# Kernel optimization log

Hardware: AMD Instinct MI355X
Metric: run time of the kernel (lower is better)

The kernel has to match this reference:

```python
import jax, jax.numpy as jnp
import numpy as np

B, S, D = 2, 2048, 2048
H, KVH = 16, 4
HD = D // H            # 128
KVD = KVH * HD         # 512
ROPE_BASE = 10000.0
EPS = 1e-6


def setup_inputs() -> dict:
    key = jax.random.key(0)
    k0, k1, k2, k3, k4, k5 = jax.random.split(key, 6)
    x = jax.random.normal(k0, (B, S, D), dtype=jnp.float32)
    # torch Linear weights are [out_features, in_features]
    Wq = jax.random.normal(k1, (D, D), dtype=jnp.float32) * 0.02
    Wk = jax.random.normal(k2, (KVD, D), dtype=jnp.float32) * 0.02
    Wv = jax.random.normal(k3, (KVD, D), dtype=jnp.float32) * 0.02
    Wproj = jax.random.normal(k4, (D, D), dtype=jnp.float32) * 0.02
    q_gain = jnp.ones((H,), dtype=jnp.float32)
    return {"x": x, "Wq": Wq, "Wk": Wk, "Wv": Wv, "Wproj": Wproj, "q_gain": q_gain}


def _rms_norm(t):
    return t * jax.lax.rsqrt(jnp.mean(t * t, axis=-1, keepdims=True) + EPS)


def _rope_tables(seqlen, dtype):
    half = HD // 2
    inv_freq = 1.0 / (ROPE_BASE ** (jnp.arange(0, HD, 2, dtype=jnp.float32) / HD))
    freqs = jnp.outer(jnp.arange(seqlen, dtype=jnp.float32), inv_freq)  # [S, half]
    return jnp.cos(freqs).astype(dtype)[None, None], jnp.sin(freqs).astype(dtype)[None, None]


def _apply_rope(t, cos, sin):
    half = t.shape[-1] // 2
    t1, t2 = t[..., :half], t[..., half:]
    return jnp.concatenate((t1 * cos + t2 * sin, -t1 * sin + t2 * cos), axis=-1)


def reference(x, Wq, Wk, Wv, Wproj, q_gain):
    bsz, seqlen, _ = x.shape
    # QKV projections (F.linear: x @ W.T)
    q = jnp.einsum('bsd,ed->bse', x, Wq).reshape(bsz, seqlen, H, HD).transpose(0, 2, 1, 3)
    k = jnp.einsum('bsd,ed->bse', x, Wk).reshape(bsz, seqlen, KVH, HD).transpose(0, 2, 1, 3)
    v = jnp.einsum('bsd,ed->bse', x, Wv).reshape(bsz, seqlen, KVH, HD).transpose(0, 2, 1, 3)
    # QK RMS-norm
    q = _rms_norm(q)
    k = _rms_norm(k)
    # RoPE
    cos, sin = _rope_tables(seqlen, q.dtype)
    q = _apply_rope(q, cos, sin)
    k = _apply_rope(k, cos, sin)
    # per-head query gain
    q = q * q_gain.astype(q.dtype)[None, :, None, None]
    # GQA: repeat_interleave kv heads
    rep = H // KVH
    k = jnp.repeat(k, rep, axis=1)
    v = jnp.repeat(v, rep, axis=1)
    # causal SDPA
    scale = 1.0 / jnp.sqrt(jnp.asarray(HD, dtype=q.dtype))
    scores = jnp.einsum('bhqd,bhkd->bhqk', q, k) * scale
    causal = jnp.tril(jnp.ones((seqlen, seqlen), dtype=bool))
    scores = jnp.where(causal[None, None], scores, jnp.finfo(scores.dtype).min)
    attn = jax.nn.softmax(scores, axis=-1)
    y = jnp.einsum('bhqk,bhkd->bhqd', attn, v)
    y = y.transpose(0, 2, 1, 3).reshape(bsz, seqlen, H * HD)
    return jnp.einsum('bse,de->bsd', y, Wproj)
```

## Files before the change

kernel.cpp:

```cpp
#include <hip/hip_runtime.h>


typedef __bf16 bf16x8 __attribute__((ext_vector_type(8)));
typedef float  f32x4  __attribute__((ext_vector_type(4)));

#define LOG2E 1.4426950408889634f
#define FIXC  16.59099297022308f

__device__ __forceinline__ float b2f(ushort h) {
  return __builtin_bit_cast(float, ((unsigned)h) << 16);
}
__device__ __forceinline__ ushort f2b(float f) {
  unsigned u = __builtin_bit_cast(unsigned, f);
  return (ushort)((u + 0x7fffu + ((u >> 16) & 1u)) >> 16);
}
__device__ __forceinline__ void async16(ushort* lds, const ushort* g) {
  __builtin_amdgcn_global_load_lds(
      (const __attribute__((address_space(1))) unsigned int*)(const void*)g,
      (__attribute__((address_space(3))) unsigned int*)(void*)lds, 16, 0, 0);
}
__device__ __forceinline__ f32x4 mfma16(bf16x8 a, bf16x8 b, f32x4 c) {
  return __builtin_amdgcn_mfma_f32_16x16x32_bf16(a, b, c, 0, 0, 0);
}

__global__ __launch_bounds__(256) void castk(const float* __restrict__ in,
                                             ushort* __restrict__ out) {
  int i = blockIdx.x * 256 + threadIdx.x;
  float4 v = ((const float4*)in)[i];
  ushort4 o = make_ushort4(f2b(v.x), f2b(v.y), f2b(v.z), f2b(v.w));
  ((ushort4*)out)[i] = o;
}

__global__ void rope_tables(float* __restrict__ cosT, float* __restrict__ sinT) {
  int s = blockIdx.x;
  int i = threadIdx.x;
  float invf = exp2f(-(float)i * (13.287712379549449f / 64.0f));
  float ang = (float)s * invf;
  float sn, cs;
  sincosf(ang, &sn, &cs);
  cosT[s * 64 + i] = cs;
  sinT[s * 64 + i] = sn;
}

__device__ __forceinline__ void store_c(float* C, size_t idx, float v) { C[idx] = v; }
__device__ __forceinline__ void store_c(ushort* C, size_t idx, float v) { C[idx] = f2b(v); }

template <typename TOUT>
__global__ __launch_bounds__(256) void gemm_bt(const ushort* __restrict__ A,
                                               const ushort* __restrict__ Bw,
                                               TOUT* __restrict__ C,
                                               int M, int N, int K) {
  __shared__ __align__(16) ushort As[128 * 32];
  __shared__ __align__(16) ushort Bs[128 * 32];
  int tid = threadIdx.x;
  int lane = tid & 63, wid = tid >> 6;
  int gx = gridDim.x;
  int nwg = gx * gridDim.y;
  int lid = blockIdx.y * gx + blockIdx.x;
  int cpx = nwg >> 3;
  int swz = (lid & 7) * cpx + (lid >> 3);
  int bm = swz / gx, bn = swz % gx;
  int wr = wid >> 1, wc = wid & 1;
  int lr = lane & 15, kg = lane >> 4;
  f32x4 z = {0.f, 0.f, 0.f, 0.f};
  f32x4 acc[4][4];
#pragma unroll
  for (int m = 0; m < 4; ++m)
#pragma unroll
    for (int n = 0; n < 4; ++n) acc[m][n] = z;

  const ushort* Ab = A + (size_t)bm * 128 * K;
  const ushort* Bb = Bw + (size_t)bn * 128 * K;
  int c0 = tid, c1 = tid + 256;

  for (int k0 = 0; k0 < K; k0 += 32) {
    async16(&As[c0 * 8], Ab + (size_t)(c0 >> 2) * K + k0 + (c0 & 3) * 8);
    async16(&As[c1 * 8], Ab + (size_t)(c1 >> 2) * K + k0 + (c1 & 3) * 8);
    async16(&Bs[c0 * 8], Bb + (size_t)(c0 >> 2) * K + k0 + (c0 & 3) * 8);
    async16(&Bs[c1 * 8], Bb + (size_t)(c1 >> 2) * K + k0 + (c1 & 3) * 8);
    __syncthreads();
    bf16x8 af[4], bfr[4];
#pragma unroll
    for (int m = 0; m < 4; ++m)
      af[m] = *(const bf16x8*)&As[(wr * 64 + m * 16 + lr) * 32 + kg * 8];
#pragma unroll
    for (int n = 0; n < 4; ++n)
      bfr[n] = *(const bf16x8*)&Bs[(wc * 64 + n * 16 + lr) * 32 + kg * 8];
#pragma unroll
    for (int m = 0; m < 4; ++m)
#pragma unroll
      for (int n = 0; n < 4; ++n)
        acc[m][n] = mfma16(af[m], bfr[n], acc[m][n]);
    __syncthreads();
  }
#pragma unroll
  for (int m = 0; m < 4; ++m)
#pragma unroll
    for (int n = 0; n < 4; ++n)
#pragma unroll
      for (int r4 = 0; r4 < 4; ++r4) {
        int row = bm * 128 + wr * 64 + m * 16 + kg * 4 + r4;
        int col = bn * 128 + wc * 64 + n * 16 + lr;
        store_c(C, (size_t)row * N + col, acc[m][n][r4]);
      }
}

__global__ __launch_bounds__(256) void rms_rope(ushort* __restrict__ qkv,
                                                const float* __restrict__ gain,
                                                const float* __restrict__ cosT,
                                                const float* __restrict__ sinT) {
  int w = blockIdx.x * 4 + (threadIdx.x >> 6);
  int lane = threadIdx.x & 63;
  int token = w / 20, slot = w % 20;
  int s = token & 2047;
  ushort* p = qkv + (size_t)token * 3072 +
              (slot < 16 ? slot * 128 : 2048 + (slot - 16) * 128);
  float t1 = b2f(p[lane]);
  float t2 = b2f(p[lane + 64]);
  float ss = t1 * t1 + t2 * t2;
#pragma unroll
  for (int off = 32; off >= 1; off >>= 1) ss += __shfl_xor(ss, off);
  float r = rsqrtf(ss * (1.0f / 128.0f) + 1e-6f);
  t1 *= r; t2 *= r;
  float c = cosT[s * 64 + lane], sn = sinT[s * 64 + lane];
  float o1 = t1 * c + t2 * sn;
  float o2 = t2 * c - t1 * sn;
  if (slot < 16) {
    float g = gain[slot] * 0.08838834764831845f;
    o1 *= g; o2 *= g;
  }
  p[lane] = f2b(o1);
  p[lane + 64] = f2b(o2);
}

__global__ __launch_bounds__(512) void attn_fwd(const ushort* __restrict__ qkv,
                                                ushort* __restrict__ y) {
  __shared__ __align__(16) ushort LDS[32768];
  ushort* Vt = LDS + 16384;
  ushort* Ps = LDS + 24576;
  ushort* Qst = LDS + 8192;

  int tid = threadIdx.x, lane = tid & 63, wid = tid >> 6;
  int lr = lane & 15, kg = lane >> 4;
  int i = blockIdx.x, bh = blockIdx.y;
  int b = bh >> 4, h = bh & 15, kvh = h >> 2;
  int lo = i, hi = 31 - i;
  size_t tokbase = (size_t)b * 2048;

  bool isHi = (wid < 4);
  int wq = isHi ? wid : (wid - 4);
  int ldsrow0 = (isHi ? 0 : 64) + wq * 16;
  int qtile = isHi ? hi : lo;
  int qbase = qtile * 64 + wq * 16;
  int nt = hi + 1;

#pragma unroll
  for (int it = 0; it < 4; ++it) {
    int c = it * 512 + tid;
    int r = c >> 4, a = c & 15;
    int asrc = a ^ (r & 7);
    int qrow = (r < 64) ? hi * 64 + r : lo * 64 + (r - 64);
    async16(&Qst[c * 8], qkv + (tokbase + qrow) * 3072 + h * 128 + asrc * 8);
  }
#pragma unroll
  for (int i2 = 0; i2 < 2; ++i2) {
    int c = i2 * 512 + tid;
    int r = c >> 4, a = c & 15;
    int asrc = a ^ (r & 7);
    async16(&LDS[c * 8], qkv + (tokbase + r) * 3072 + 2048 + kvh * 128 + asrc * 8);
  }
  int vkv0 = tid >> 4, vd0 = (tid & 15) * 8;
  uint4 va = *(const uint4*)(qkv + (tokbase + vkv0) * 3072 + 2560 + kvh * 128 + vd0);
  uint4 vb_ = *(const uint4*)(qkv + (tokbase + 32 + vkv0) * 3072 + 2560 + kvh * 128 + vd0);

  __syncthreads();

  bf16x8 qf[4];
#pragma unroll
  for (int kk = 0; kk < 4; ++kk) {
    int r = ldsrow0 + lr;
    int a = (kk * 4 + kg) ^ (r & 7);
    qf[kk] = *(const bf16x8*)&Qst[r * 128 + a * 8];
  }
  __syncthreads();

  f32x4 z = {0.f, 0.f, 0.f, 0.f};
  f32x4 acc_y[8];
#pragma unroll
  for (int n2 = 0; n2 < 8; ++n2) acc_y[n2] = z;
  float lsum[4] = {0.f, 0.f, 0.f, 0.f};

  for (int t = 0; t < nt; ++t) {
    ushort* kb = LDS + ((t & 1) ? 8192 : 0);
#pragma unroll
    for (int i2 = 0; i2 < 2; ++i2) {
      union { uint4 u; ushort s[8]; } vv;
      vv.u = i2 ? vb_ : va;
      int kv = i2 * 32 + vkv0;
#pragma unroll
      for (int j = 0; j < 8; ++j) {
        int d = vd0 + j;
        int sw = (d & 7) ^ ((d >> 3) & 7);
        Vt[d * 64 + (kv ^ (sw << 3))] = vv.s[j];
      }
    }
    __syncthreads();

    if (t + 1 < nt) {
      ushort* kn = LDS + (((t + 1) & 1) ? 8192 : 0);
      int ktn = (t + 1) * 64;
#pragma unroll
      for (int i2 = 0; i2 < 2; ++i2) {
        int c = i2 * 512 + tid;
        int r = c >> 4, a = c & 15;
        int asrc = a ^ (r & 7);
        async16(&kn[c * 8],
                qkv + (tokbase + ktn + r) * 3072 + 2048 + kvh * 128 + asrc * 8);
      }
      va  = *(const uint4*)(qkv + (tokbase + ktn + vkv0) * 3072 + 2560 + kvh * 128 + vd0);
      vb_ = *(const uint4*)(qkv + (tokbase + ktn + 32 + vkv0) * 3072 + 2560 + kvh * 128 + vd0);
    }

    bool act = isHi || (t <= lo);
    if (act) {
      int kt = t * 64;
      f32x4 sc[4];
#pragma unroll
      for (int n = 0; n < 4; ++n) sc[n] = z;
      __builtin_amdgcn_s_setprio(1);
#pragma unroll
      for (int n = 0; n < 4; ++n)
#pragma unroll
        for (int kk = 0; kk < 4; ++kk) {
          int r = n * 16 + lr;
          int a = (kk * 4 + kg) ^ (r & 7);
          bf16x8 kf = *(const bf16x8*)&kb[r * 128 + a * 8];
          sc[n] = mfma16(qf[kk], kf, sc[n]);
        }
      __builtin_amdgcn_s_setprio(0);
      if (t == qtile) {
#pragma unroll
        for (int n = 0; n < 4; ++n)
#pragma unroll
          for (int r4 = 0; r4 < 4; ++r4) {
            int kvg = kt + n * 16 + lr;
            int qg = qbase + kg * 4 + r4;
            if (kvg > qg) sc[n][r4] = -1.0e30f;
          }
      }
#pragma unroll
      for (int n = 0; n < 4; ++n)
#pragma unroll
        for (int r4 = 0; r4 < 4; ++r4) {
          float pv = __builtin_amdgcn_exp2f(fmaf(sc[n][r4], LOG2E, -FIXC));
          lsum[r4] += pv;
          int q = ldsrow0 + kg * 4 + r4;
          int col = n * 16 + lr;
          Ps[q * 64 + (col ^ ((q & 7) << 3))] = f2b(pv);
        }
      bf16x8 pa[2];
#pragma unroll
      for (int kk2 = 0; kk2 < 2; ++kk2) {
        int q = ldsrow0 + lr;
        pa[kk2] = *(const bf16x8*)&Ps[q * 64 + ((kk2 * 32 + kg * 8) ^ ((q & 7) << 3))];
      }
      __builtin_amdgcn_s_setprio(1);
#pragma unroll
      for (int n2 = 0; n2 < 8; ++n2) {
        int d = n2 * 16 + lr;
        int sw = (d & 7) ^ ((d >> 3) & 7);
#pragma unroll
        for (int kk2 = 0; kk2 < 2; ++kk2) {
          bf16x8 vb = *(const bf16x8*)&Vt[d * 64 + ((kk2 * 32 + kg * 8) ^ (sw << 3))];
          acc_y[n2] = mfma16(pa[kk2], vb, acc_y[n2]);
        }
      }
      __builtin_amdgcn_s_setprio(0);
    }
    __syncthreads();
  }

#pragma unroll
  for (int off = 1; off < 16; off <<= 1)
#pragma unroll
    for (int r4 = 0; r4 < 4; ++r4) lsum[r4] += __shfl_xor(lsum[r4], off);
  float rl[4];
#pragma unroll
  for (int r4 = 0; r4 < 4; ++r4) rl[r4] = 1.0f / lsum[r4];
#pragma unroll
  for (int n2 = 0; n2 < 8; ++n2)
#pragma unroll
    for (int r4 = 0; r4 < 4; ++r4) {
      int q = qbase + kg * 4 + r4;
      float v = acc_y[n2][r4] * rl[r4];
      y[(tokbase + q) * 2048 + h * 128 + n2 * 16 + lr] = f2b(v);
    }
}

extern "C" void kernel_launch(void* const* d_in, const int* in_sizes, int n_in,
                              void* d_out, int out_size, void* d_ws, size_t ws_size,
                              hipStream_t stream) {
  const float* x  = (const float*)d_in[0];
  const float* Wq = (const float*)d_in[1];
  const float* Wk = (const float*)d_in[2];
  const float* Wv = (const float*)d_in[3];
  const float* Wp = (const float*)d_in[4];
  const float* qg = (const float*)d_in[5];
  float* out = (float*)d_out;

  char* w = (char*)d_ws;
  ushort* xb    = (ushort*)w; w += (size_t)4096 * 2048 * 2;
  ushort* wqkv  = (ushort*)w; w += (size_t)3072 * 2048 * 2;
  ushort* wproj = (ushort*)w; w += (size_t)2048 * 2048 * 2;
  ushort* qkv   = (ushort*)w; w += (size_t)4096 * 3072 * 2;
  ushort* yb    = (ushort*)w; w += (size_t)4096 * 2048 * 2;
  float*  cosT  = (float*)w;  w += (size_t)2048 * 64 * 4;
  float*  sinT  = (float*)w;  w += (size_t)2048 * 64 * 4;

  castk<<<8192, 256, 0, stream>>>(x, xb);
  castk<<<4096, 256, 0, stream>>>(Wq, wqkv);
  castk<<<1024, 256, 0, stream>>>(Wk, wqkv + (size_t)2048 * 2048);
  castk<<<1024, 256, 0, stream>>>(Wv, wqkv + (size_t)2560 * 2048);
  castk<<<4096, 256, 0, stream>>>(Wp, wproj);
  rope_tables<<<2048, 64, 0, stream>>>(cosT, sinT);

  gemm_bt<ushort><<<dim3(24, 32), 256, 0, stream>>>(xb, wqkv, qkv, 4096, 3072, 2048);
  rms_rope<<<20480, 256, 0, stream>>>(qkv, qg, cosT, sinT);
  attn_fwd<<<dim3(16, 32), 512, 0, stream>>>(qkv, yb);
  gemm_bt<float><<<dim3(16, 32), 256, 0, stream>>>(yb, wproj, out, 4096, 2048, 2048);
}
```

Before: 364.6 us.

## Split high-tile KV work across idle waves and widen GEMM K-step with swizzle

In attention, once the low query tile has finished its KV range, its waves switch to the high query tile and take the odd KV tiles of each pair in parallel with the other waves. The two partial outputs and row sums are then merged through LDS, which balances work across all eight waves instead of leaving half of them idle. The GEMM now stages 64-wide K chunks with an XOR-swizzled LDS layout, halving the number of barriers per K and reducing bank conflicts. The cost is more LDS (two V buffers), more registers for a second accumulator set, and a merge step at the end. Q is now loaded straight from global memory instead of being staged through LDS.

New measurement: 344.1 us. 1.06x faster.

```diff
diff --git a/kernel.cpp b/kernel.cpp
--- a/kernel.cpp
+++ b/kernel.cpp
@@ -50,8 +50,8 @@
                                                const ushort* __restrict__ Bw,
                                                TOUT* __restrict__ C,
                                                int M, int N, int K) {
-  __shared__ __align__(16) ushort As[128 * 32];
-  __shared__ __align__(16) ushort Bs[128 * 32];
+  __shared__ __align__(16) ushort As[128 * 64];
+  __shared__ __align__(16) ushort Bs[128 * 64];
   int tid = threadIdx.x;
   int lane = tid & 63, wid = tid >> 6;
   int gx = gridDim.x;
@@ -71,26 +71,41 @@
 
   const ushort* Ab = A + (size_t)bm * 128 * K;
   const ushort* Bb = Bw + (size_t)bn * 128 * K;
-  int c0 = tid, c1 = tid + 256;
-
-  for (int k0 = 0; k0 < K; k0 += 32) {
-    async16(&As[c0 * 8], Ab + (size_t)(c0 >> 2) * K + k0 + (c0 & 3) * 8);
-    async16(&As[c1 * 8], Ab + (size_t)(c1 >> 2) * K + k0 + (c1 & 3) * 8);
-    async16(&Bs[c0 * 8], Bb + (size_t)(c0 >> 2) * K + k0 + (c0 & 3) * 8);
-    async16(&Bs[c1 * 8], Bb + (size_t)(c1 >> 2) * K + k0 + (c1 & 3) * 8);
-    __syncthreads();
-    bf16x8 af[4], bfr[4];
+
+  for (int k0 = 0; k0 < K; k0 += 64) {
+#pragma unroll
+    for (int p = 0; p < 4; ++p) {
+      int c = p * 256 + tid;
+      int r = c >> 3, ch = c & 7;
+      int chs = ch ^ (r & 7);
+      async16(&As[c * 8], Ab + (size_t)r * K + k0 + chs * 8);
+      async16(&Bs[c * 8], Bb + (size_t)r * K + k0 + chs * 8);
+    }
+    __syncthreads();
+    bf16x8 af[4][2], bfr[4][2];
 #pragma unroll
     for (int m = 0; m < 4; ++m)
-      af[m] = *(const bf16x8*)&As[(wr * 64 + m * 16 + lr) * 32 + kg * 8];
+#pragma unroll
+      for (int kk = 0; kk < 2; ++kk) {
+        int r = wr * 64 + m * 16 + lr;
+        int a = (kk * 4 + kg) ^ (r & 7);
+        af[m][kk] = *(const bf16x8*)&As[r * 64 + a * 8];
+      }
 #pragma unroll
     for (int n = 0; n < 4; ++n)
-      bfr[n] = *(const bf16x8*)&Bs[(wc * 64 + n * 16 + lr) * 32 + kg * 8];
+#pragma unroll
+      for (int kk = 0; kk < 2; ++kk) {
+        int r = wc * 64 + n * 16 + lr;
+        int a = (kk * 4 + kg) ^ (r & 7);
+        bfr[n][kk] = *(const bf16x8*)&Bs[r * 64 + a * 8];
+      }
 #pragma unroll
     for (int m = 0; m < 4; ++m)
 #pragma unroll
       for (int n = 0; n < 4; ++n)
-        acc[m][n] = mfma16(af[m], bfr[n], acc[m][n]);
+#pragma unroll
+        for (int kk = 0; kk < 2; ++kk)
+          acc[m][n] = mfma16(af[m][kk], bfr[n][kk], acc[m][n]);
     __syncthreads();
   }
 #pragma unroll
@@ -133,12 +148,73 @@
   p[lane + 64] = f2b(o2);
 }
 
+__device__ __forceinline__ void compute_tile(
+    const ushort* __restrict__ kb, const ushort* __restrict__ vt,
+    ushort* __restrict__ Ps, const bf16x8 (&qf)[4],
+    f32x4 (&acc)[8], float (&ls)[4],
+    int lr, int kg, int ldsrow0, bool domask, int kt, int qr0) {
+  f32x4 z = {0.f, 0.f, 0.f, 0.f};
+  f32x4 sc[4];
+#pragma unroll
+  for (int n = 0; n < 4; ++n) sc[n] = z;
+  __builtin_amdgcn_s_setprio(1);
+#pragma unroll
+  for (int n = 0; n < 4; ++n)
+#pragma unroll
+    for (int kk = 0; kk < 4; ++kk) {
+      int r = n * 16 + lr;
+      int a = (kk * 4 + kg) ^ (r & 7);
+      bf16x8 kf = *(const bf16x8*)&kb[r * 128 + a * 8];
+      sc[n] = mfma16(qf[kk], kf, sc[n]);
+    }
+  __builtin_amdgcn_s_setprio(0);
+  if (domask) {
+#pragma unroll
+    for (int n = 0; n < 4; ++n)
+#pragma unroll
+      for (int r4 = 0; r4 < 4; ++r4) {
+        int kvg = kt + n * 16 + lr;
+        int qg = qr0 + kg * 4 + r4;
+        if (kvg > qg) sc[n][r4] = -1.0e30f;
+      }
+  }
+#pragma unroll
+  for (int n = 0; n < 4; ++n)
+#pragma unroll
+    for (int r4 = 0; r4 < 4; ++r4) {
+      float pv = __builtin_amdgcn_exp2f(fmaf(sc[n][r4], LOG2E, -FIXC));
+      ls[r4] += pv;
+      int q = ldsrow0 + kg * 4 + r4;
+      int col = n * 16 + lr;
+      Ps[q * 64 + (col ^ ((q & 7) << 3))] = f2b(pv);
+    }
+  bf16x8 pa0, pa1;
+  {
+    int q = ldsrow0 + lr;
+    pa0 = *(const bf16x8*)&Ps[q * 64 + ((kg * 8) ^ ((q & 7) << 3))];
+    pa1 = *(const bf16x8*)&Ps[q * 64 + ((32 + kg * 8) ^ ((q & 7) << 3))];
+  }
+  __builtin_amdgcn_s_setprio(1);
+#pragma unroll
+  for (int n2 = 0; n2 < 8; ++n2) {
+    int d = n2 * 16 + lr;
+    int sw = (d & 7) ^ ((d >> 3) & 7);
+    bf16x8 v0 = *(const bf16x8*)&vt[d * 64 + ((kg * 8) ^ (sw << 3))];
+    acc[n2] = mfma16(pa0, v0, acc[n2]);
+    bf16x8 v1 = *(const bf16x8*)&vt[d * 64 + ((32 + kg * 8) ^ (sw << 3))];
+    acc[n2] = mfma16(pa1, v1, acc[n2]);
+  }
+  __builtin_amdgcn_s_setprio(0);
+}
+
 __global__ __launch_bounds__(512) void attn_fwd(const ushort* __restrict__ qkv,
                                                 ushort* __restrict__ y) {
-  __shared__ __align__(16) ushort LDS[32768];
-  ushort* Vt = LDS + 16384;
-  ushort* Ps = LDS + 24576;
-  ushort* Qst = LDS + 8192;
+  __shared__ __align__(16) ushort LDS[40960];
+  ushort* K0 = LDS;
+  ushort* K1 = LDS + 8192;
+  ushort* V0 = LDS + 16384;
+  ushort* V1 = LDS + 24576;
+  ushort* Ps = LDS + 32768;
 
   int tid = threadIdx.x, lane = tid & 63, wid = tid >> 6;
   int lr = lane & 15, kg = lane >> 4;
@@ -147,154 +223,157 @@
   int lo = i, hi = 31 - i;
   size_t tokbase = (size_t)b * 2048;
 
-  bool isHi = (wid < 4);
-  int wq = isHi ? wid : (wid - 4);
-  int ldsrow0 = (isHi ? 0 : 64) + wq * 16;
-  int qtile = isHi ? hi : lo;
-  int qbase = qtile * 64 + wq * 16;
-  int nt = hi + 1;
-
-#pragma unroll
-  for (int it = 0; it < 4; ++it) {
-    int c = it * 512 + tid;
-    int r = c >> 4, a = c & 15;
-    int asrc = a ^ (r & 7);
-    int qrow = (r < 64) ? hi * 64 + r : lo * 64 + (r - 64);
-    async16(&Qst[c * 8], qkv + (tokbase + qrow) * 3072 + h * 128 + asrc * 8);
-  }
-#pragma unroll
-  for (int i2 = 0; i2 < 2; ++i2) {
-    int c = i2 * 512 + tid;
-    int r = c >> 4, a = c & 15;
-    int asrc = a ^ (r & 7);
-    async16(&LDS[c * 8], qkv + (tokbase + r) * 3072 + 2048 + kvh * 128 + asrc * 8);
-  }
+  bool w03 = (wid < 4);
+  int g = wid & 3;
+  int ldsrow0 = (w03 ? 0 : 64) + g * 16;
+  int qr0A = (w03 ? hi : lo) * 64 + g * 16;
+  int qr0B = hi * 64 + g * 16;
+
   int vkv0 = tid >> 4, vd0 = (tid & 15) * 8;
-  uint4 va = *(const uint4*)(qkv + (tokbase + vkv0) * 3072 + 2560 + kvh * 128 + vd0);
-  uint4 vb_ = *(const uint4*)(qkv + (tokbase + 32 + vkv0) * 3072 + 2560 + kvh * 128 + vd0);
-
+  uint4 va, vb_;
+
+#define STAGE_K(BUF, T)                                                      \
+  {                                                                          \
+    _Pragma("unroll") for (int i2 = 0; i2 < 2; ++i2) {                       \
+      int c = i2 * 512 + tid;                                                \
+      int r = c >> 4, a = c & 15;                                            \
+      int asrc = a ^ (r & 7);                                                \
+      async16(&(BUF)[c * 8],                                                 \
+              qkv + (tokbase + (size_t)(T) * 64 + r) * 3072 + 2048 +         \
+                  kvh * 128 + asrc * 8);                                     \
+    }                                                                        \
+  }
+#define LOAD_V(T)                                                            \
+  {                                                                          \
+    va = *(const uint4*)(qkv + (tokbase + (size_t)(T) * 64 + vkv0) * 3072 +  \
+                         2560 + kvh * 128 + vd0);                            \
+    vb_ = *(const uint4*)(qkv +                                              \
+                          (tokbase + (size_t)(T) * 64 + 32 + vkv0) * 3072 +  \
+                          2560 + kvh * 128 + vd0);                           \
+  }
+#define WRITE_V(VB)                                                          \
+  {                                                                          \
+    union { uint4 u; ushort s[8]; } vv0, vv1;                                \
+    vv0.u = va; vv1.u = vb_;                                                 \
+    _Pragma("unroll") for (int j = 0; j < 8; ++j) {                          \
+      int d = vd0 + j;                                                       \
+      int sw = (d & 7) ^ ((d >> 3) & 7);                                     \
+      (VB)[d * 64 + (vkv0 ^ (sw << 3))] = vv0.s[j];                          \
+      (VB)[d * 64 + ((32 + vkv0) ^ (sw << 3))] = vv1.s[j];                   \
+    }                                                                        \
+  }
+
+  bf16x8 qf[4];
+#pragma unroll
+  for (int kk = 0; kk < 4; ++kk)
+    qf[kk] = *(const bf16x8*)(qkv + (tokbase + qr0A + lr) * 3072 + h * 128 +
+                              (kk * 4 + kg) * 8);
+
+  f32x4 z = {0.f, 0.f, 0.f, 0.f};
+  f32x4 acc_y[8], acc2[8];
+#pragma unroll
+  for (int n2 = 0; n2 < 8; ++n2) { acc_y[n2] = z; acc2[n2] = z; }
+  float lsum[4] = {0.f, 0.f, 0.f, 0.f};
+  float lsum2[4] = {0.f, 0.f, 0.f, 0.f};
+
+  STAGE_K(K0, 0);
+  LOAD_V(0);
+
+  for (int s = 0; s <= lo; ++s) {
+    ushort* kb = (s & 1) ? K1 : K0;
+    ushort* vt = (s & 1) ? V1 : V0;
+    WRITE_V(vt);
+    __syncthreads();
+    if (s < lo) {
+      STAGE_K(((s & 1) ? K0 : K1), s + 1);
+      LOAD_V(s + 1);
+    }
+    compute_tile(kb, vt, Ps, qf, acc_y, lsum, lr, kg, ldsrow0,
+                 (!w03 && s == lo), s * 64, qr0A);
+    __syncthreads();
+  }
+
+  if (!w03) {
+#pragma unroll
+    for (int kk = 0; kk < 4; ++kk)
+      qf[kk] = *(const bf16x8*)(qkv + (tokbase + qr0B + lr) * 3072 + h * 128 +
+                                (kk * 4 + kg) * 8);
+  }
+
+  int mmax = 15 - i;
+  for (int m = 0; m <= mmax; ++m) {
+    int t0 = lo + 1 + 2 * m;
+    bool has1 = (t0 + 1 <= hi);
+    LOAD_V(t0);
+    STAGE_K(K0, t0);
+    if (has1) STAGE_K(K1, t0 + 1);
+    WRITE_V(V0);
+    if (has1) {
+      LOAD_V(t0 + 1);
+      WRITE_V(V1);
+    }
+    __syncthreads();
+    if (w03) {
+      compute_tile(K0, V0, Ps, qf, acc_y, lsum, lr, kg, ldsrow0,
+                   (t0 == hi), t0 * 64, qr0B);
+    } else if (has1) {
+      compute_tile(K1, V1, Ps, qf, acc2, lsum2, lr, kg, ldsrow0,
+                   false, (t0 + 1) * 64, qr0B);
+    }
+    __syncthreads();
+  }
+
+#pragma unroll
+  for (int off = 1; off < 16; off <<= 1)
+#pragma unroll
+    for (int r4 = 0; r4 < 4; ++r4) {
+      lsum[r4] += __shfl_xor(lsum[r4], off);
+      lsum2[r4] += __shfl_xor(lsum2[r4], off);
+    }
+
+  float* scf = (float*)LDS;
+  float* scl = (float*)(LDS + 16384);
+  if (!w03) {
+#pragma unroll
+    for (int n2 = 0; n2 < 8; ++n2)
+#pragma unroll
+      for (int r4 = 0; r4 < 4; ++r4)
+        scf[(g * 16 + kg * 4 + r4) * 128 + n2 * 16 + lr] = acc2[n2][r4];
+#pragma unroll
+    for (int r4 = 0; r4 < 4; ++r4)
+      if (lr == r4) scl[g * 16 + kg * 4 + r4] = lsum2[r4];
+  }
   __syncthreads();
 
-  bf16x8 qf[4];
-#pragma unroll
-  for (int kk = 0; kk < 4; ++kk) {
-    int r = ldsrow0 + lr;
-    int a = (kk * 4 + kg) ^ (r & 7);
-    qf[kk] = *(const bf16x8*)&Qst[r * 128 + a * 8];
-  }
-  __syncthreads();
-
-  f32x4 z = {0.f, 0.f, 0.f, 0.f};
-  f32x4 acc_y[8];
-#pragma unroll
-  for (int n2 = 0; n2 < 8; ++n2) acc_y[n2] = z;
-  float lsum[4] = {0.f, 0.f, 0.f, 0.f};
-
-  for (int t = 0; t < nt; ++t) {
-    ushort* kb = LDS + ((t & 1) ? 8192 : 0);
-#pragma unroll
-    for (int i2 = 0; i2 < 2; ++i2) {
-      union { uint4 u; ushort s[8]; } vv;
-      vv.u = i2 ? vb_ : va;
-      int kv = i2 * 32 + vkv0;
-#pragma unroll
-      for (int j = 0; j < 8; ++j) {
-        int d = vd0 + j;
-        int sw = (d & 7) ^ ((d >> 3) & 7);
-        Vt[d * 64 + (kv ^ (sw << 3))] = vv.s[j];
-      }
-    }
-    __syncthreads();
-
-    if (t + 1 < nt) {
-      ushort* kn = LDS + (((t + 1) & 1) ? 8192 : 0);
-      int ktn = (t + 1) * 64;
-#pragma unroll
-      for (int i2 = 0; i2 < 2; ++i2) {
-        int c = i2 * 512 + tid;
-        int r = c >> 4, a = c & 15;
-        int asrc = a ^ (r & 7);
-        async16(&kn[c * 8],
-                qkv + (tokbase + ktn + r) * 3072 + 2048 + kvh * 128 + asrc * 8);
-      }
-      va  = *(const uint4*)(qkv + (tokbase + ktn + vkv0) * 3072 + 2560 + kvh * 128 + vd0);
-      vb_ = *(const uint4*)(qkv + (tokbase + ktn + 32 + vkv0) * 3072 + 2560 + kvh * 128 + vd0);
-    }
-
-    bool act = isHi || (t <= lo);
-    if (act) {
-      int kt = t * 64;
-      f32x4 sc[4];
-#pragma unroll
-      for (int n = 0; n < 4; ++n) sc[n] = z;
-      __builtin_amdgcn_s_setprio(1);
-#pragma unroll
-      for (int n = 0; n < 4; ++n)
-#pragma unroll
-        for (int kk = 0; kk < 4; ++kk) {
-          int r = n * 16 + lr;
-          int a = (kk * 4 + kg) ^ (r & 7);
-          bf16x8 kf = *(const bf16x8*)&kb[r * 128 + a * 8];
-          sc[n] = mfma16(qf[kk], kf, sc[n]);
-        }
-      __builtin_amdgcn_s_setprio(0);
-      if (t == qtile) {
-#pragma unroll
-        for (int n = 0; n < 4; ++n)
-#pragma unroll
-          for (int r4 = 0; r4 < 4; ++r4) {
-            int kvg = kt + n * 16 + lr;
-            int qg = qbase + kg * 4 + r4;
-            if (kvg > qg) sc[n][r4] = -1.0e30f;
-          }
-      }
-#pragma unroll
-      for (int n = 0; n < 4; ++n)
-#pragma unroll
-        for (int r4 = 0; r4 < 4; ++r4) {
-          float pv = __builtin_amdgcn_exp2f(fmaf(sc[n][r4], LOG2E, -FIXC));
-          lsum[r4] += pv;
-          int q = ldsrow0 + kg * 4 + r4;
-          int col = n * 16 + lr;
-          Ps[q * 64 + (col ^ ((q & 7) << 3))] = f2b(pv);
-        }
-      bf16x8 pa[2];
-#pragma unroll
-      for (int kk2 = 0; kk2 < 2; ++kk2) {
-        int q = ldsrow0 + lr;
-        pa[kk2] = *(const bf16x8*)&Ps[q * 64 + ((kk2 * 32 + kg * 8) ^ ((q & 7) << 3))];
-      }
-      __builtin_amdgcn_s_setprio(1);
-#pragma unroll
-      for (int n2 = 0; n2 < 8; ++n2) {
-        int d = n2 * 16 + lr;
-        int sw = (d & 7) ^ ((d >> 3) & 7);
-#pragma unroll
-        for (int kk2 = 0; kk2 < 2; ++kk2) {
-          bf16x8 vb = *(const bf16x8*)&Vt[d * 64 + ((kk2 * 32 + kg * 8) ^ (sw << 3))];
-          acc_y[n2] = mfma16(pa[kk2], vb, acc_y[n2]);
-        }
-      }
-      __builtin_amdgcn_s_setprio(0);
-    }
-    __syncthreads();
-  }
-
-#pragma unroll
-  for (int off = 1; off < 16; off <<= 1)
-#pragma unroll
-    for (int r4 = 0; r4 < 4; ++r4) lsum[r4] += __shfl_xor(lsum[r4], off);
-  float rl[4];
-#pragma unroll
-  for (int r4 = 0; r4 < 4; ++r4) rl[r4] = 1.0f / lsum[r4];
-#pragma unroll
-  for (int n2 = 0; n2 < 8; ++n2)
-#pragma unroll
-    for (int r4 = 0; r4 < 4; ++r4) {
-      int q = qbase + kg * 4 + r4;
-      float v = acc_y[n2][r4] * rl[r4];
-      y[(tokbase + q) * 2048 + h * 128 + n2 * 16 + lr] = f2b(v);
-    }
+  if (w03) {
+    float rl[4];
+#pragma unroll
+    for (int r4 = 0; r4 < 4; ++r4)
+      rl[r4] = 1.0f / (lsum[r4] + scl[wid * 16 + kg * 4 + r4]);
+#pragma unroll
+    for (int n2 = 0; n2 < 8; ++n2)
+#pragma unroll
+      for (int r4 = 0; r4 < 4; ++r4) {
+        int row = wid * 16 + kg * 4 + r4;
+        float v = (acc_y[n2][r4] + scf[row * 128 + n2 * 16 + lr]) * rl[r4];
+        y[(tokbase + hi * 64 + row) * 2048 + h * 128 + n2 * 16 + lr] = f2b(v);
+      }
+  } else {
+    float rl[4];
+#pragma unroll
+    for (int r4 = 0; r4 < 4; ++r4) rl[r4] = 1.0f / lsum[r4];
+#pragma unroll
+    for (int n2 = 0; n2 < 8; ++n2)
+#pragma unroll
+      for (int r4 = 0; r4 < 4; ++r4) {
+        int row = g * 16 + kg * 4 + r4;
+        float v = acc_y[n2][r4] * rl[r4];
+        y[(tokbase + lo * 64 + row) * 2048 + h * 128 + n2 * 16 + lr] = f2b(v);
+      }
+  }
+#undef STAGE_K
+#undef LOAD_V
+#undef WRITE_V
 }
 
 extern "C" void kernel_launch(void* const* d_in, const int* in_sizes, int n_in,
```

## Rewrite attention with 32x32 MFMA split-KV work sharing; widen GEMM K tile

Applied to the files above, without the earlier changes.

The attention kernel drops from 512 to 256 threads and uses 32x32x16 MFMA with 32 query rows per wave. The softmax probabilities are passed between lanes in registers through shuffles instead of going through LDS. Causal work is balanced by having all four waves first process the low tile. The high tile's remaining KV blocks are then split between wave pairs and their partial accumulators merged through LDS. Separately, the GEMM K-step grows to 64 with an XOR-swizzled LDS layout, which halves the barriers per K and reduces bank conflicts at the cost of more LDS per block.

Result: slower. 377.3 us (+3.5%).

```diff
diff --git a/kernel.cpp b/kernel.cpp
--- a/kernel.cpp
+++ b/kernel.cpp
@@ -3,6 +3,7 @@
 
 typedef __bf16 bf16x8 __attribute__((ext_vector_type(8)));
 typedef float  f32x4  __attribute__((ext_vector_type(4)));
+typedef float  f32x16 __attribute__((ext_vector_type(16)));
 
 #define LOG2E 1.4426950408889634f
 #define FIXC  16.59099297022308f
@@ -21,6 +22,9 @@
 }
 __device__ __forceinline__ f32x4 mfma16(bf16x8 a, bf16x8 b, f32x4 c) {
   return __builtin_amdgcn_mfma_f32_16x16x32_bf16(a, b, c, 0, 0, 0);
+}
+__device__ __forceinline__ f32x16 mfma32(bf16x8 a, bf16x8 b, f32x16 c) {
+  return __builtin_amdgcn_mfma_f32_32x32x16_bf16(a, b, c, 0, 0, 0);
 }
 
 __global__ __launch_bounds__(256) void castk(const float* __restrict__ in,
@@ -50,8 +54,8 @@
                                                const ushort* __restrict__ Bw,
                                                TOUT* __restrict__ C,
                                                int M, int N, int K) {
-  __shared__ __align__(16) ushort As[128 * 32];
-  __shared__ __align__(16) ushort Bs[128 * 32];
+  __shared__ __align__(16) ushort As[128 * 64];
+  __shared__ __align__(16) ushort Bs[128 * 64];
   int tid = threadIdx.x;
   int lane = tid & 63, wid = tid >> 6;
   int gx = gridDim.x;
@@ -71,26 +75,41 @@
 
   const ushort* Ab = A + (size_t)bm * 128 * K;
   const ushort* Bb = Bw + (size_t)bn * 128 * K;
-  int c0 = tid, c1 = tid + 256;
-
-  for (int k0 = 0; k0 < K; k0 += 32) {
-    async16(&As[c0 * 8], Ab + (size_t)(c0 >> 2) * K + k0 + (c0 & 3) * 8);
-    async16(&As[c1 * 8], Ab + (size_t)(c1 >> 2) * K + k0 + (c1 & 3) * 8);
-    async16(&Bs[c0 * 8], Bb + (size_t)(c0 >> 2) * K + k0 + (c0 & 3) * 8);
-    async16(&Bs[c1 * 8], Bb + (size_t)(c1 >> 2) * K + k0 + (c1 & 3) * 8);
+
+  for (int k0 = 0; k0 < K; k0 += 64) {
+#pragma unroll
+    for (int p = 0; p < 4; ++p) {
+      int c = p * 256 + tid;
+      int r = c >> 3, ch = c & 7;
+      int chs = ch ^ (r & 7);
+      async16(&As[c * 8], Ab + (size_t)r * K + k0 + chs * 8);
+      async16(&Bs[c * 8], Bb + (size_t)r * K + k0 + chs * 8);
+    }
     __syncthreads();
-    bf16x8 af[4], bfr[4];
+    bf16x8 af[4][2], bfr[4][2];
 #pragma unroll
     for (int m = 0; m < 4; ++m)
-      af[m] = *(const bf16x8*)&As[(wr * 64 + m * 16 + lr) * 32 + kg * 8];
+#pragma unroll
+      for (int kk = 0; kk < 2; ++kk) {
+        int r = wr * 64 + m * 16 + lr;
+        int a = (kk * 4 + kg) ^ (r & 7);
+        af[m][kk] = *(const bf16x8*)&As[r * 64 + a * 8];
+      }
 #pragma unroll
     for (int n = 0; n < 4; ++n)
-      bfr[n] = *(const bf16x8*)&Bs[(wc * 64 + n * 16 + lr) * 32 + kg * 8];
+#pragma unroll
+      for (int kk = 0; kk < 2; ++kk) {
+        int r = wc * 64 + n * 16 + lr;
+        int a = (kk * 4 + kg) ^ (r & 7);
+        bfr[n][kk] = *(const bf16x8*)&Bs[r * 64 + a * 8];
+      }
 #pragma unroll
     for (int m = 0; m < 4; ++m)
 #pragma unroll
       for (int n = 0; n < 4; ++n)
-        acc[m][n] = mfma16(af[m], bfr[n], acc[m][n]);
+#pragma unroll
+        for (int kk = 0; kk < 2; ++kk)
+          acc[m][n] = mfma16(af[m][kk], bfr[n][kk], acc[m][n]);
     __syncthreads();
   }
 #pragma unroll
@@ -133,168 +152,225 @@
   p[lane + 64] = f2b(o2);
 }
 
-__global__ __launch_bounds__(512) void attn_fwd(const ushort* __restrict__ qkv,
+__global__ __launch_bounds__(256) void attn_fwd(const ushort* __restrict__ qkv,
                                                 ushort* __restrict__ y) {
   __shared__ __align__(16) ushort LDS[32768];
-  ushort* Vt = LDS + 16384;
-  ushort* Ps = LDS + 24576;
-  ushort* Qst = LDS + 8192;
-
-  int tid = threadIdx.x, lane = tid & 63, wid = tid >> 6;
-  int lr = lane & 15, kg = lane >> 4;
-  int i = blockIdx.x, bh = blockIdx.y;
-  int b = bh >> 4, h = bh & 15, kvh = h >> 2;
-  int lo = i, hi = 31 - i;
-  size_t tokbase = (size_t)b * 2048;
-
-  bool isHi = (wid < 4);
-  int wq = isHi ? wid : (wid - 4);
-  int ldsrow0 = (isHi ? 0 : 64) + wq * 16;
-  int qtile = isHi ? hi : lo;
-  int qbase = qtile * 64 + wq * 16;
-  int nt = hi + 1;
-
-#pragma unroll
-  for (int it = 0; it < 4; ++it) {
-    int c = it * 512 + tid;
-    int r = c >> 4, a = c & 15;
-    int asrc = a ^ (r & 7);
-    int qrow = (r < 64) ? hi * 64 + r : lo * 64 + (r - 64);
-    async16(&Qst[c * 8], qkv + (tokbase + qrow) * 3072 + h * 128 + asrc * 8);
-  }
-#pragma unroll
-  for (int i2 = 0; i2 < 2; ++i2) {
-    int c = i2 * 512 + tid;
-    int r = c >> 4, a = c & 15;
-    int asrc = a ^ (r & 7);
-    async16(&LDS[c * 8], qkv + (tokbase + r) * 3072 + 2048 + kvh * 128 + asrc * 8);
-  }
-  int vkv0 = tid >> 4, vd0 = (tid & 15) * 8;
-  uint4 va = *(const uint4*)(qkv + (tokbase + vkv0) * 3072 + 2560 + kvh * 128 + vd0);
-  uint4 vb_ = *(const uint4*)(qkv + (tokbase + 32 + vkv0) * 3072 + 2560 + kvh * 128 + vd0);
-
+  ushort* K0 = LDS;
+  ushort* K1 = LDS + 8192;
+  ushort* V0 = LDS + 16384;
+  ushort* V1 = LDS + 24576;
+
+  const int tid = threadIdx.x;
+  const int lane = tid & 63;
+  const int w = tid >> 6;
+  const int hf = lane >> 5;
+  const int lq = lane & 31;
+  const int i = blockIdx.x, bh = blockIdx.y;
+  const int b = bh >> 4, h = bh & 15, kvh = h >> 2;
+  const int ta = i, tb = 31 - i;
+  const size_t tokbase = (size_t)b * 2048;
+  const bool isW01 = (w < 2);
+  const int sub = isW01 ? w : (w - 2);
+
+  const int kv0 = (tid & 15) * 4;
+  const int d0 = (tid >> 4) * 8;
+
+  union U16 { uint4 u; ushort s[8]; };
+  U16 vA[4], vB[4];
+
+  auto LOADV = [&](U16 (&vr)[4], int T) {
+#pragma unroll
+    for (int l = 0; l < 4; ++l)
+      vr[l].u = *(const uint4*)(qkv + (tokbase + (size_t)T * 64 + kv0 + l) * 3072 +
+                                2560 + kvh * 128 + d0);
+  };
+  auto WRITEV = [&](ushort* VB, U16 (&vr)[4]) {
+#pragma unroll
+    for (int j = 0; j < 8; ++j) {
+      int row = d0 + j;
+      int ad = row * 64 + ((((kv0 >> 3) ^ (row & 7)) << 3) | (kv0 & 7));
+      *(ushort4*)&VB[ad] = make_ushort4(vr[0].s[j], vr[1].s[j], vr[2].s[j], vr[3].s[j]);
+    }
+  };
+  auto STAGEK = [&](ushort* KB, int T) {
+#pragma unroll
+    for (int it = 0; it < 4; ++it) {
+      int c = it * 256 + tid;
+      int r = c >> 4, a = c & 15;
+      int asrc = a ^ (r & 15);
+      async16(&KB[c * 8],
+              qkv + (tokbase + (size_t)T * 64 + r) * 3072 + 2048 + kvh * 128 + asrc * 8);
+    }
+  };
+
+  bf16x8 qf[8];
+  auto LOADQ = [&](int qrow0) {
+#pragma unroll
+    for (int kk = 0; kk < 8; ++kk)
+      qf[kk] = *(const bf16x8*)(qkv + (tokbase + qrow0 + lq) * 3072 + h * 128 +
+                                kk * 16 + hf * 8);
+  };
+
+  const f32x16 Z16 = {0.f,0.f,0.f,0.f,0.f,0.f,0.f,0.f,0.f,0.f,0.f,0.f,0.f,0.f,0.f,0.f};
+  f32x16 acc[4];
+#pragma unroll
+  for (int db = 0; db < 4; ++db) acc[db] = Z16;
+  float lsum = 0.f;
+
+  auto COMPUTE = [&](const ushort* kb, const ushort* vt, bool domask, int kvbase, int qg) {
+#pragma unroll
+    for (int kvb = 0; kvb < 2; ++kvb) {
+      f32x16 sc = Z16;
+      __builtin_amdgcn_s_setprio(1);
+#pragma unroll
+      for (int kk = 0; kk < 8; ++kk) {
+        int kv = kvb * 32 + lq;
+        int ch = (2 * kk + hf) ^ (kv & 15);
+        bf16x8 kf = *(const bf16x8*)&kb[kv * 128 + ch * 8];
+        sc = mfma32(kf, qf[kk], sc);
+      }
+      __builtin_amdgcn_s_setprio(0);
+      if (domask) {
+#pragma unroll
+        for (int r = 0; r < 16; ++r) {
+          int kvl = (r & 3) + 8 * (r >> 2) + 4 * hf;
+          if (kvbase + kvb * 32 + kvl > qg) sc[r] = -1.0e30f;
+        }
+      }
+      float ex[16];
+#pragma unroll
+      for (int r = 0; r < 16; ++r) ex[r] = __shfl_xor(sc[r], 32);
+#pragma unroll
+      for (int c2 = 0; c2 < 2; ++c2) {
+        bf16x8 pa;
+#pragma unroll
+        for (int j = 0; j < 8; ++j) {
+          int r0 = 8 * c2 + (j & 3);
+          int r1 = r0 + 4;
+          float v0 = (j < 4) ? sc[r0] : ex[r0];
+          float v1 = (j < 4) ? ex[r1] : sc[r1];
+          float v = hf ? v1 : v0;
+          float p = __builtin_amdgcn_exp2f(fmaf(v, LOG2E, -FIXC));
+          lsum += p;
+          pa[j] = __builtin_bit_cast(__bf16, f2b(p));
+        }
+        int kkpv = 2 * kvb + c2;
+        __builtin_amdgcn_s_setprio(1);
+#pragma unroll
+        for (int db = 0; db < 4; ++db) {
+          int d = db * 32 + lq;
+          int ch = (2 * kkpv + hf) ^ (d & 7);
+          bf16x8 vbf = *(const bf16x8*)&vt[d * 64 + ch * 8];
+          acc[db] = mfma32(pa, vbf, acc[db]);
+        }
+        __builtin_amdgcn_s_setprio(0);
+      }
+    }
+  };
+
+  auto STOREO = [&](size_t rowbase, float lf) {
+    float rl = 1.0f / lf;
+#pragma unroll
+    for (int r = 0; r < 16; ++r) {
+      int q2 = (r & 3) + 8 * (r >> 2) + 4 * hf;
+      float rlq = __shfl(rl, q2);
+#pragma unroll
+      for (int db = 0; db < 4; ++db) {
+        int d = db * 32 + lq;
+        y[(rowbase + q2) * 2048 + h * 128 + d] = f2b(acc[db][r] * rlq);
+      }
+    }
+  };
+
+  const int qrowA = (isW01 ? tb : ta) * 64 + sub * 32;
+  const int qgA = qrowA + lq;
+  LOADQ(qrowA);
+
+  LOADV(vA, 0);
+  STAGEK(K0, 0);
+  WRITEV(V0, vA);
   __syncthreads();
 
-  bf16x8 qf[4];
-#pragma unroll
-  for (int kk = 0; kk < 4; ++kk) {
-    int r = ldsrow0 + lr;
-    int a = (kk * 4 + kg) ^ (r & 7);
-    qf[kk] = *(const bf16x8*)&Qst[r * 128 + a * 8];
+  for (int t = 0; t <= ta; ++t) {
+    ushort* kb = (t & 1) ? K1 : K0;
+    ushort* vb = (t & 1) ? V1 : V0;
+    bool more = (t < ta);
+    if (more) {
+      STAGEK((t & 1) ? K0 : K1, t + 1);
+      LOADV(vA, t + 1);
+    }
+    COMPUTE(kb, vb, (!isW01 && t == ta), t * 64, qgA);
+    if (more) WRITEV((t & 1) ? V0 : V1, vA);
+    __syncthreads();
+  }
+
+  if (!isW01) {
+    float lf = lsum + __shfl_xor(lsum, 32);
+    STOREO(tokbase + (size_t)ta * 64 + sub * 32, lf);
+#pragma unroll
+    for (int db = 0; db < 4; ++db) acc[db] = Z16;
+    lsum = 0.f;
+    LOADQ(tb * 64 + sub * 32);
+  }
+  const int qgB = tb * 64 + sub * 32 + lq;
+
+  {
+    int t0 = ta + 1;
+    bool h1 = (t0 + 1 <= tb);
+    STAGEK(K0, t0);
+    if (h1) STAGEK(K1, t0 + 1);
+    LOADV(vA, t0);
+    if (h1) LOADV(vB, t0 + 1);
+    WRITEV(V0, vA);
+    if (h1) WRITEV(V1, vB);
   }
   __syncthreads();
 
-  f32x4 z = {0.f, 0.f, 0.f, 0.f};
-  f32x4 acc_y[8];
-#pragma unroll
-  for (int n2 = 0; n2 < 8; ++n2) acc_y[n2] = z;
-  float lsum[4] = {0.f, 0.f, 0.f, 0.f};
-
-  for (int t = 0; t < nt; ++t) {
-    ushort* kb = LDS + ((t & 1) ? 8192 : 0);
-#pragma unroll
-    for (int i2 = 0; i2 < 2; ++i2) {
-      union { uint4 u; ushort s[8]; } vv;
-      vv.u = i2 ? vb_ : va;
-      int kv = i2 * 32 + vkv0;
-#pragma unroll
-      for (int j = 0; j < 8; ++j) {
-        int d = vd0 + j;
-        int sw = (d & 7) ^ ((d >> 3) & 7);
-        Vt[d * 64 + (kv ^ (sw << 3))] = vv.s[j];
-      }
+  for (int m = 0;; ++m) {
+    int t0 = ta + 1 + 2 * m, t1 = t0 + 1;
+    bool has1 = (t1 <= tb);
+    bool morePairs = (t0 + 2 <= tb);
+    bool more1 = (t0 + 3 <= tb);
+    if (morePairs) {
+      LOADV(vA, t0 + 2);
+      if (more1) LOADV(vB, t0 + 3);
+    }
+    if (isW01) {
+      COMPUTE(K0, V0, (t0 == tb), t0 * 64, qgB);
+    } else if (has1) {
+      COMPUTE(K1, V1, false, t1 * 64, qgB);
     }
     __syncthreads();
-
-    if (t + 1 < nt) {
-      ushort* kn = LDS + (((t + 1) & 1) ? 8192 : 0);
-      int ktn = (t + 1) * 64;
-#pragma unroll
-      for (int i2 = 0; i2 < 2; ++i2) {
-        int c = i2 * 512 + tid;
-        int r = c >> 4, a = c & 15;
-        int asrc = a ^ (r & 7);
-        async16(&kn[c * 8],
-                qkv + (tokbase + ktn + r) * 3072 + 2048 + kvh * 128 + asrc * 8);
-      }
-      va  = *(const uint4*)(qkv + (tokbase + ktn + vkv0) * 3072 + 2560 + kvh * 128 + vd0);
-      vb_ = *(const uint4*)(qkv + (tokbase + ktn + 32 + vkv0) * 3072 + 2560 + kvh * 128 + vd0);
-    }
-
-    bool act = isHi || (t <= lo);
-    if (act) {
-      int kt = t * 64;
-      f32x4 sc[4];
-#pragma unroll
-      for (int n = 0; n < 4; ++n) sc[n] = z;
-      __builtin_amdgcn_s_setprio(1);
-#pragma unroll
-      for (int n = 0; n < 4; ++n)
-#pragma unroll
-        for (int kk = 0; kk < 4; ++kk) {
-          int r = n * 16 + lr;
-          int a = (kk * 4 + kg) ^ (r & 7);
-          bf16x8 kf = *(const bf16x8*)&kb[r * 128 + a * 8];
-          sc[n] = mfma16(qf[kk], kf, sc[n]);
-        }
-      __builtin_amdgcn_s_setprio(0);
-      if (t == qtile) {
-#pragma unroll
-        for (int n = 0; n < 4; ++n)
-#pragma unroll
-          for (int r4 = 0; r4 < 4; ++r4) {
-            int kvg = kt + n * 16 + lr;
-            int qg = qbase + kg * 4 + r4;
-            if (kvg > qg) sc[n][r4] = -1.0e30f;
-          }
-      }
-#pragma unroll
-      for (int n = 0; n < 4; ++n)
-#pragma unroll
-        for (int r4 = 0; r4 < 4; ++r4) {
-          float pv = __builtin_amdgcn_exp2f(fmaf(sc[n][r4], LOG2E, -FIXC));
-          lsum[r4] += pv;
-          int q = ldsrow0 + kg * 4 + r4;
-          int col = n * 16 + lr;
-          Ps[q * 64 + (col ^ ((q & 7) << 3))] = f2b(pv);
-        }
-      bf16x8 pa[2];
-#pragma unroll
-      for (int kk2 = 0; kk2 < 2; ++kk2) {
-        int q = ldsrow0 + lr;
-        pa[kk2] = *(const bf16x8*)&Ps[q * 64 + ((kk2 * 32 + kg * 8) ^ ((q & 7) << 3))];
-      }
-      __builtin_amdgcn_s_setprio(1);
-#pragma unroll
-      for (int n2 = 0; n2 < 8; ++n2) {
-        int d = n2 * 16 + lr;
-        int sw = (d & 7) ^ ((d >> 3) & 7);
-#pragma unroll
-        for (int kk2 = 0; kk2 < 2; ++kk2) {
-          bf16x8 vb = *(const bf16x8*)&Vt[d * 64 + ((kk2 * 32 + kg * 8) ^ (sw << 3))];
-          acc_y[n2] = mfma16(pa[kk2], vb, acc_y[n2]);
-        }
-      }
-      __builtin_amdgcn_s_setprio(0);
-    }
+    if (!morePairs) break;
+    STAGEK(K0, t0 + 2);
+    if (more1) STAGEK(K1, t0 + 3);
+    WRITEV(V0, vA);
+    if (more1) WRITEV(V1, vB);
     __syncthreads();
   }
 
-#pragma unroll
-  for (int off = 1; off < 16; off <<= 1)
-#pragma unroll
-    for (int r4 = 0; r4 < 4; ++r4) lsum[r4] += __shfl_xor(lsum[r4], off);
-  float rl[4];
-#pragma unroll
-  for (int r4 = 0; r4 < 4; ++r4) rl[r4] = 1.0f / lsum[r4];
-#pragma unroll
-  for (int n2 = 0; n2 < 8; ++n2)
-#pragma unroll
-    for (int r4 = 0; r4 < 4; ++r4) {
-      int q = qbase + kg * 4 + r4;
-      float v = acc_y[n2][r4] * rl[r4];
-      y[(tokbase + q) * 2048 + h * 128 + n2 * 16 + lr] = f2b(v);
-    }
+  float* scf = (float*)LDS;
+  if (!isW01) {
+    float lf = lsum + __shfl_xor(lsum, 32);
+    int p = sub;
+#pragma unroll
+    for (int db = 0; db < 4; ++db)
+#pragma unroll
+      for (int r = 0; r < 16; ++r)
+        scf[p * 4096 + (db * 16 + r) * 64 + lane] = acc[db][r];
+    scf[8192 + p * 64 + lane] = lf;
+  }
+  __syncthreads();
+  if (isW01) {
+    int p = sub;
+#pragma unroll
+    for (int db = 0; db < 4; ++db)
+#pragma unroll
+      for (int r = 0; r < 16; ++r)
+        acc[db][r] += scf[p * 4096 + (db * 16 + r) * 64 + lane];
+    float lf = lsum + __shfl_xor(lsum, 32) + scf[8192 + p * 64 + lane];
+    STOREO(tokbase + (size_t)tb * 64 + sub * 32, lf);
+  }
 }
 
 extern "C" void kernel_launch(void* const* d_in, const int* in_sizes, int n_in,
@@ -326,6 +402,6 @@
 
   gemm_bt<ushort><<<dim3(24, 32), 256, 0, stream>>>(xb, wqkv, qkv, 4096, 3072, 2048);
   rms_rope<<<20480, 256, 0, stream>>>(qkv, qg, cosT, sinT);
-  attn_fwd<<<dim3(16, 32), 512, 0, stream>>>(qkv, yb);
+  attn_fwd<<<dim3(16, 32), 256, 0, stream>>>(qkv, yb);
   gemm_bt<float><<<dim3(16, 32), 256, 0, stream>>>(yb, wproj, out, 4096, 2048, 2048);
 }
```
